# Performance work log

Measured on AMD Instinct MI355X. Metric: run time of the kernel, lower is better.

The kernel has to match this reference:

```python
import jax, jax.numpy as jnp
import numpy as np

L = 4        # number of GCN layers
B = 1024     # batch of brain graphs
R = 116      # ROIs (AAL atlas)
EPS = 1e-5   # BatchNorm eps


def setup_inputs() -> dict:
    key = jax.random.key(0)
    ks = jax.random.split(key, 20)
    def rn(k, shape, scale=0.1):
        return jax.random.normal(k, shape, dtype=jnp.float32) * scale
    return {
        "X": jax.random.normal(ks[0], (B, R, 3), dtype=jnp.float32),
        "Z": jax.random.normal(ks[1], (B, R, R), dtype=jnp.float32),
        "aw1": rn(ks[2], (L, 3, 3)), "ab1": rn(ks[3], (L, 3)),
        "aw2": rn(ks[4], (L, R, R)), "ab2": rn(ks[5], (L, R)),
        "nw": rn(ks[6], (L, 3, 3)), "nb": rn(ks[7], (L, 3)),
        "ew": rn(ks[8], (L, R, R)), "eb": rn(ks[9], (L, R)),
        "gn_g": jnp.ones((L, R), jnp.float32), "gn_b": jnp.zeros((L, R), jnp.float32),
        "ge_g": jnp.ones((L, R), jnp.float32), "ge_b": jnp.zeros((L, R), jnp.float32),
        "dn_w": rn(ks[10], (L + 1, 3)), "dn_b": rn(ks[11], (L + 1,)),
        "dn_g": jnp.ones((L + 1,), jnp.float32), "dn_beta": jnp.zeros((L + 1,), jnp.float32),
        "de_w": rn(ks[12], (L + 1, 78)), "de_b": rn(ks[13], (L + 1,)),
        "de_g": jnp.ones((L + 1,), jnp.float32), "de_beta": jnp.zeros((L + 1,), jnp.float32),
        "cw1": rn(ks[14], (1024, R * 4 * (L + 1)), 0.02), "cb1": jnp.zeros((1024,), jnp.float32),
        "cw2": rn(ks[15], (2, 1024), 0.02), "cb2": jnp.zeros((2,), jnp.float32),
    }


def _bn3(x, g, b):
    # BatchNorm1d(C) in training mode on (N, C, L): stats over (N, L) per channel
    m = x.mean(axis=(0, 2), keepdims=True)
    v = x.var(axis=(0, 2), keepdims=True)
    return (x - m) * jax.lax.rsqrt(v + EPS) * g[None, :, None] + b[None, :, None]


def _down_node(X, w, b, g, beta):
    # ConvDownSample(3): Conv1d(1,1,3) on (B*R,1,3) -> scalar per row, ReLU, BatchNorm1d(1)
    f = jax.nn.relu(X.reshape(-1, 3) @ w + b)                 # (B*R,)
    h = (f - f.mean()) * jax.lax.rsqrt(f.var() + EPS) * g + beta
    return h.reshape(X.shape[0], -1)                          # (B, R)


def _down_edge(Z, w, b, g, beta):
    # ConvDownSample(116): Conv1d(1,1,78,stride=39,pad=39) -> 3 outputs per row
    x = Z.reshape(-1, R)
    xp = jnp.pad(x, ((0, 0), (39, 39)))                       # (B*R, 194)
    win = jnp.stack([xp[:, 39 * t: 39 * t + 78] for t in range(3)], axis=1)  # (B*R,3,78)
    f = jax.nn.relu(win @ w + b)                              # (B*R, 3)
    h = (f - f.mean()) * jax.lax.rsqrt(f.var() + EPS) * g + beta
    return h.reshape(Z.shape[0], -1)                          # (B, 3R)


def reference(X, Z, aw1, ab1, aw2, ab2, nw, nb, ew, eb, gn_g, gn_b, ge_g, ge_b,
              dn_w, dn_b, dn_g, dn_beta, de_w, de_b, de_g, de_beta,
              cw1, cb1, cw2, cb2):
    xx = [_down_node(X, dn_w[0], dn_b[0], dn_g[0], dn_beta[0])]
    zz = [_down_edge(Z, de_w[0], de_b[0], de_g[0], de_beta[0])]
    for i in range(L):
        # Attention: K = conv1(X^T) (1x1 conv == matmul), Q = K^T, scores = Q@K
        K = jnp.einsum('oc,bnc->bon', aw1[i], X) + ab1[i][None, :, None]   # (B,3,R)
        att = jax.nn.softmax(jnp.einsum('bcn,bcm->bnm', K, K), axis=-1)    # (B,R,R)
        V = jnp.einsum('oc,bmc->bom', aw2[i], Z) + ab2[i][None, :, None]   # (B,R,R)
        A = jnp.einsum('bnk,bkm->bmn', att, V)                             # bmm + permute
        # Edge update
        Z1 = jnp.einsum('bnm,bmc->bnc', A, Z) @ ew[i].T + eb[i]
        Z = jax.nn.relu(_bn3(Z1, ge_g[i], ge_b[i])) + Z
        zz.append(_down_edge(Z, de_w[i + 1], de_b[i + 1], de_g[i + 1], de_beta[i + 1]))
        # Node update
        X1 = jnp.einsum('bnm,bmc->bnc', A, X) @ nw[i].T + nb[i]
        X = jax.nn.relu(_bn3(X1, gn_g[i], gn_b[i])) + X
        xx.append(_down_node(X, dn_w[i + 1], dn_b[i + 1], dn_g[i + 1], dn_beta[i + 1]))
    XZ = jnp.concatenate(xx + zz, axis=1)                     # (B, 116*4*(L+1))
    h = jax.nn.relu(XZ @ cw1.T + cb1)                         # dropout is identity (eval)
    return h @ cw2.T + cb2                                    # (B, 2)
```

## Files before the change

### kernel.cpp

```cpp
#include <hip/hip_runtime.h>
#if __has_include(<hip/hip_bf16.h>)
#include <hip/hip_bf16.h>
#define HAVE_HIP_BF16 1
#endif

#define R 116
#define RP 120
#define GZ 13920
#define BATCH 1024
#define NL 4
#define RR2 13456
#define EPSF 1e-5f
#define NZP_ELEM (BATCH * GZ)
#define NZ_ELEM (BATCH * RR2)
#define NX_ELEM (BATCH * R * 3)
#define LS 136
#define XZS 2336
#define NSH 8
#define STL 464
#define NCHP 1740

typedef unsigned short ushort_t;
typedef __attribute__((ext_vector_type(8))) short bf16x8;
typedef __attribute__((ext_vector_type(4))) float f32x4;

__device__ __forceinline__ float bf2f(unsigned short u){
  union { unsigned int i; float f; } v; v.i = ((unsigned int)u) << 16; return v.f;
}
__device__ __forceinline__ unsigned short f2bf(float f){
#ifdef HAVE_HIP_BF16
  union { __hip_bfloat16 h; unsigned short u; } cv;
  cv.h = __float2bfloat16(f);
  return cv.u;
#else
  union { float ff; unsigned int i; } v; v.ff = f;
  return (unsigned short)((v.i + 0x7fffu + ((v.i >> 16) & 1u)) >> 16);
#endif
}
__device__ __forceinline__ float u2f_lo(unsigned w){
  union { unsigned i; float f; } v; v.i = w << 16; return v.f;
}
__device__ __forceinline__ float u2f_hi(unsigned w){
  union { unsigned i; float f; } v; v.i = w & 0xffff0000u; return v.f;
}
__device__ __forceinline__ float wsum(float v){
  #pragma unroll
  for (int o = 32; o > 0; o >>= 1) v += __shfl_xor(v, o, 64);
  return v;
}
__device__ __forceinline__ float wmaxr(float v){
  #pragma unroll
  for (int o = 32; o > 0; o >>= 1) v = fmaxf(v, __shfl_xor(v, o, 64));
  return v;
}

__global__ void k_init(const float* __restrict__ Zin, ushort_t* __restrict__ Zcp,
                       const float* __restrict__ Xin, float* __restrict__ Xc,
                       float* __restrict__ st, unsigned* __restrict__ xzw,
                       unsigned* __restrict__ z1g,
                       const float* __restrict__ aw2, const float* __restrict__ ew,
                       ushort_t* __restrict__ aw2p, ushort_t* __restrict__ ewp,
                       const float* __restrict__ cw1, ushort_t* __restrict__ cw1p,
                       const float* __restrict__ cb2, float* __restrict__ out)
{
  int idx = blockIdx.x * 256 + threadIdx.x;
  int stride = gridDim.x * 256;
  for (int i = idx; i < BATCH * NCHP; i += stride){
    int g = i / NCHP, ch = i - g * NCHP;
    int e0 = ch << 3, r = e0 / RP, c0 = e0 - r * RP;
    const float* zi = Zin + (size_t)g * RR2 + r * R + c0;
    float4 f0 = *(const float4*)zi;
    uint4 w;
    w.x = (unsigned)f2bf(f0.x) | ((unsigned)f2bf(f0.y) << 16);
    w.y = (unsigned)f2bf(f0.z) | ((unsigned)f2bf(f0.w) << 16);
    if (c0 == 112){ w.z = 0u; w.w = 0u; }
    else {
      float4 f1 = *(const float4*)(zi + 4);
      w.z = (unsigned)f2bf(f1.x) | ((unsigned)f2bf(f1.y) << 16);
      w.w = (unsigned)f2bf(f1.z) | ((unsigned)f2bf(f1.w) << 16);
    }
    *(uint4*)(Zcp + (size_t)g * GZ + e0) = w;
  }
  for (int i = idx; i < 1024 * XZS; i += stride){
    int n = i / XZS, k = i - n * XZS;
    cw1p[i] = (k < 2320) ? f2bf(cw1[n*2320 + k]) : (ushort_t)0;
  }
  for (int i = idx; i < 4*128*128; i += stride){
    int l = i >> 14, rem = i & 16383, row = rem >> 7, col = rem & 127;
    ushort_t v = 0, w = 0;
    if (row < R && col < R){
      v = f2bf(aw2[l*RR2 + col*R + row]);
      w = f2bf(ew [l*RR2 + row*R + col]);
    }
    aw2p[i] = v;
    ewp [i] = w;
  }
  for (int i = idx; i < NX_ELEM; i += stride) Xc[i] = Xin[i];
  for (int i = idx; i < 15008; i += stride) st[i] = 0.f;
  for (int i = idx; i < BATCH*XZS/2; i += stride) xzw[i] = 0u;
  for (int i = idx; i < 736; i += stride) z1g[i] = 0u;
  for (int i = idx; i < 1024; i += stride){ out[2*i] = cb2[0]; out[2*i+1] = cb2[1]; }
}

__launch_bounds__(1024, 8)
__global__ void k_fused(float* __restrict__ Xc, ushort_t* __restrict__ Zc,
                        ushort_t* __restrict__ Z1, float* __restrict__ X1,
                        const float* __restrict__ aw1, const float* __restrict__ ab1,
                        const ushort_t* __restrict__ aw2p, const float* __restrict__ ab2,
                        const float* __restrict__ nw,  const float* __restrict__ nb,
                        const ushort_t* __restrict__ ewp,  const float* __restrict__ eb,
                        float* __restrict__ zsumS, float* __restrict__ zsqS,
                        float* __restrict__ xsumS, float* __restrict__ xsqS,
                        const float* __restrict__ geg, const float* __restrict__ geb,
                        const float* __restrict__ gng, const float* __restrict__ gnb,
                        const float* __restrict__ dnw, const float* __restrict__ dnb,
                        const float* __restrict__ dew, const float* __restrict__ deb,
                        ushort_t* __restrict__ XZ,
                        float* __restrict__ dnS, float* __restrict__ deS,
                        int layer, int with_attn)
{
  __shared__ __align__(16) ushort_t bA[128*LS];
  __shared__ __align__(16) ushort_t bB[128*LS];
  __shared__ float Ksm[3*R];
  __shared__ float ssm[R];
  __shared__ float xp[R*12];
  __shared__ float zps[128*2];
  __shared__ float zpq[128*2];
  __shared__ float wsm[78];
  __shared__ float xsred[3], xqred[3];
  __shared__ float zds[8], zqs[8];

  float* zcoA = xp;
  float* zcoC = xp + 116;
  float* xcoA = xp + 232;
  float* xcoC = xp + 348;
  ushort_t* bBlin = bB;

  const int b    = blockIdx.x;
  const int tid  = threadIdx.x;
  const int lane = tid & 63;
  const int wave = tid >> 6;
  const int qm   = lane & 15;
  const int quad = lane >> 4;
  const int tr   = wave & 7;
  const int tc0  = (wave >> 3) * 4;
  const int t_snap = layer;
  const int sh   = b & (NSH-1);

  ushort_t* Zb = Zc + (size_t)b * GZ;
  const ushort_t* Z1b = Z1 + (size_t)b * RR2;
  const float* ab2l = ab2 + layer * R;
  const float* ebl  = eb  + layer * R;
  const float* nwl  = nw  + layer * 9;
  const float* nbl  = nb  + layer * 3;
  const ushort_t* aw2l = aw2p + layer * 16384;
  const ushort_t* ewl  = ewp  + layer * 16384;

  const f32x4 vzero = {0.f, 0.f, 0.f, 0.f};

  if (tid < R){
    float a = 0.f, c = 0.f;
    if (layer > 0){
      const int pl = layer - 1;
      float ms = 0.f, qs = 0.f;
      #pragma unroll
      for (int s2 = 0; s2 < NSH; s2++){
        ms += zsumS[s2*STL + pl*R + tid];
        qs += zsqS [s2*STL + pl*R + tid];
      }
      const float cnt = (float)(BATCH * R);
      float m  = ms / cnt;
      float va = fmaxf(qs / cnt - m*m, 0.f);
      float rs = rsqrtf(va + EPSF);
      a = rs * geg[pl*R + tid];
      c = geb[pl*R + tid] - m * a;
    }
    zcoA[tid] = a; zcoC[tid] = c;
  } else if (tid >= 128 && tid < 128 + R){
    const int r = tid - 128;
    float a = 0.f, c = 0.f;
    if (layer > 0){
      const int pl = layer - 1;
      float ms = 0.f, qs = 0.f;
      #pragma unroll
      for (int s2 = 0; s2 < NSH; s2++){
        ms += xsumS[s2*STL + pl*R + r];
        qs += xsqS [s2*STL + pl*R + r];
      }
      const float cnt = (float)(BATCH * 3);
      float m  = ms / cnt;
      float va = fmaxf(qs / cnt - m*m, 0.f);
      float rs = rsqrtf(va + EPSF);
      a = rs * gng[pl*R + r];
      c = gnb[pl*R + r] - m * a;
    }
    xcoA[r] = a; xcoC[r] = c;
  } else if (tid >= 256 && tid < 256 + 78){
    wsm[tid - 256] = dew[t_snap*78 + (tid - 256)];
  }
  __syncthreads();

  {
    const int ch0 = tid;
    const int ch1 = tid + 1024;
    const bool hasB = (ch1 < NCHP);
    const int e0A = ch0 << 3;
    const int e0B = ch1 << 3;
    uint4 zcA = *(const uint4*)(Zb + e0A);
    uint4 zcB; if (hasB) zcB = *(const uint4*)(Zb + e0B);
    if (layer > 0){
      const int rA = e0A / RP, cA0 = e0A - rA*RP;
      const int rB = hasB ? (e0B / RP) : 0, cB0 = hasB ? (e0B - rB*RP) : 0;
      const ushort_t* z1pA = Z1b + rA*R + cA0;
      const ushort_t* z1pB = Z1b + rB*R + cB0;
      unsigned z1A[4], z1B[4];
      #pragma unroll
      for (int i = 0; i < 4; i++) z1A[i] = *(const unsigned*)(z1pA + 2*i);
      if (hasB){
        #pragma unroll
        for (int i = 0; i < 4; i++) z1B[i] = *(const unsigned*)(z1pB + 2*i);
      }
      #pragma unroll
      for (int half = 0; half < 2; half++){
        if (half == 1 && !hasB) break;
        const int e0 = half ? e0B : e0A;
        const int r  = half ? rB  : rA;
        const int c0 = half ? cB0 : cA0;
        const uint4 zc4 = half ? zcB : zcA;
        const unsigned* z1w = half ? z1B : z1A;
        const float aa = zcoA[r], cc = zcoC[r];
        const unsigned zw[4] = {zc4.x, zc4.y, zc4.z, zc4.w};
        unsigned ow[4];
        #pragma unroll
        for (int h = 0; h < 4; h++){
          float vL = fmaxf(u2f_lo(z1w[h])*aa + cc, 0.f) + u2f_lo(zw[h]);
          float vH = fmaxf(u2f_hi(z1w[h])*aa + cc, 0.f) + u2f_hi(zw[h]);
          ow[h] = (unsigned)f2bf(vL) | ((unsigned)f2bf(vH) << 16);
        }
        if (c0 == 112){ ow[2] = 0u; ow[3] = 0u; }
        uint4 o; o.x = ow[0]; o.y = ow[1]; o.z = ow[2]; o.w = ow[3];
        if (with_attn) *(uint4*)(Zb + e0) = o;
        *(uint4*)&bBlin[e0] = o;
      }
    } else {
      *(uint4*)&bBlin[e0A] = zcA;
      if (hasB) *(uint4*)&bBlin[e0B] = zcB;
    }
  }
  {
    float fv = 0.f;
    if (tid >= 658 && tid < 658 + R){
      const int u = tid - 658;
      float* xcr = Xc + ((size_t)b*R + u)*3;
      float v0, v1, v2;
      if (layer > 0){
        float a = xcoA[u], c = xcoC[u];
        const float* x1r = X1 + ((size_t)b*R + u)*3;
        v0 = fmaxf(x1r[0]*a + c, 0.f) + xcr[0];
        v1 = fmaxf(x1r[1]*a + c, 0.f) + xcr[1];
        v2 = fmaxf(x1r[2]*a + c, 0.f) + xcr[2];
        if (with_attn){ xcr[0] = v0; xcr[1] = v1; xcr[2] = v2; }
      } else {
        v0 = xcr[0]; v1 = xcr[1]; v2 = xcr[2];
      }
      if (with_attn){
        const float* aw1l = aw1 + layer * 9;
        const float* ab1l = ab1 + layer * 3;
        #pragma unroll
        for (int o = 0; o < 3; o++)
          Ksm[o*R + u] = ab1l[o] + aw1l[o*3+0]*v0 + aw1l[o*3+1]*v1 + aw1l[o*3+2]*v2;
      }
      float f = fmaxf(dnw[t_snap*3+0]*v0 + dnw[t_snap*3+1]*v1 + dnw[t_snap*3+2]*v2 + dnb[t_snap], 0.f);
      XZ[(size_t)b*XZS + t_snap*R + u] = f2bf(f);
      fv = f;
    }
    if (wave >= 10 && wave <= 12){
      float s = wsum(fv), q = wsum(fv*fv);
      if (lane == 0){ xsred[wave - 10] = s; xqred[wave - 10] = q; }
    }
  }
  if (tid >= 774){
    for (int i = tid - 774; i < 12*LS; i += 250) bA[116*LS + i] = 0;
    for (int i = tid - 774; i < 116*20; i += 250){
      int r = i/20, c = 116 + (i - r*20);
      bA[r*LS + c] = 0;
    }
  }
  __syncthreads();

  if (wave < 10){
    if (tid == 0){
      atomicAdd(&dnS[sh*10 + t_snap*2+0], xsred[0] + xsred[1] + xsred[2]);
      atomicAdd(&dnS[sh*10 + t_snap*2+1], xqred[0] + xqred[1] + xqred[2]);
    }
    if (with_attn){
      for (int n = wave; n < R; n += 10){
        float k0 = Ksm[n], k1 = Ksm[R+n], k2 = Ksm[2*R+n];
        int m0 = lane, m1 = lane + 64;
        float a0 = k0*Ksm[m0] + k1*Ksm[R+m0] + k2*Ksm[2*R+m0];
        float a1 = (m1 < R) ? (k0*Ksm[m1] + k1*Ksm[R+m1] + k2*Ksm[2*R+m1]) : -1e30f;
        float mx = wmaxr(fmaxf(a0, a1));
        float e0 = __expf(a0 - mx);
        float e1 = (m1 < R) ? __expf(a1 - mx) : 0.f;
        float sm = wsum(e0 + e1);
        float sab = wsum(e0 * ab2l[m0] + ((m1 < R) ? e1 * ab2l[m1] : 0.f));
        float inv = 1.f / sm;
        bA[n*LS + m0] = f2bf(e0 * inv);
        if (m1 < R) bA[n*LS + m1] = f2bf(e1 * inv);
        if (lane == 0) ssm[n] = sab * inv;
      }
    }
  } else {
    const int u = tid - 640;
    float f = 0.f;
    if (u < 348){
      int r = u / 3, w = u - 3*r;
      int jlo = (w == 0) ? 39 : 0;
      int jhi = (w == 2) ? 77 : 78;
      int off = (w - 1) * 39;
      const ushort_t* vr = &bBlin[r*RP];
      float acc = 0.f;
      for (int j = jlo; j < jhi; j++) acc += wsm[j] * bf2f(vr[j + off]);
      f = fmaxf(acc + deb[t_snap], 0.f);
      XZ[(size_t)b*XZS + 5*R + t_snap*3*R + r*3 + w] = f2bf(f);
    }
    float s = wsum(f), q = wsum(f*f);
    if (lane == 0){ zds[wave - 10] = s; zqs[wave - 10] = q; }
  }
  __syncthreads();

  if (tid == 0){
    float ss = 0.f, qq = 0.f;
    #pragma unroll
    for (int k = 0; k < 6; k++){ ss += zds[k]; qq += zqs[k]; }
    atomicAdd(&deS[sh*10 + t_snap*2+0], ss);
    atomicAdd(&deS[sh*10 + t_snap*2+1], qq);
  }
  if (!with_attn) return;

  {
    f32x4 acc[4];
    #pragma unroll
    for (int t = 0; t < 4; t++) acc[t] = vzero;
    for (int kk = 0; kk < 128; kk += 32){
      bf16x8 a = *(const bf16x8*)(aw2l + (tr*16 + qm)*128 + kk + quad*8);
      #pragma unroll
      for (int t = 0; t < 4; t++){
        bf16x8 bf = *(const bf16x8*)&bA[((tc0 + t)*16 + qm)*LS + kk + quad*8];
        acc[t] = __builtin_amdgcn_mfma_f32_16x16x32_bf16(a, bf, acc[t], 0, 0, 0);
      }
    }
    const int r0 = tr*16 + quad*4;
    #pragma unroll
    for (int t = 0; t < 4; t++){
      int nn = (tc0 + t)*16 + qm;
      uint2 w;
      w.x = (unsigned)f2bf(acc[t][0]) | ((unsigned)f2bf(acc[t][1]) << 16);
      w.y = (unsigned)f2bf(acc[t][2]) | ((unsigned)f2bf(acc[t][3]) << 16);
      *(uint2*)&bB[nn*LS + r0] = w;
    }
  }
  __syncthreads();

  {
    f32x4 acc[4];
    #pragma unroll
    for (int t = 0; t < 4; t++) acc[t] = vzero;
    for (int kk = 0; kk < 128; kk += 32){
      bf16x8 a = *(const bf16x8*)&bB[(tr*16 + qm)*LS + kk + quad*8];
      #pragma unroll
      for (int t = 0; t < 4; t++){
        int nn = (tc0 + t)*16 + qm;
        bf16x8 bf = *(const bf16x8*)(Zb + nn*RP + kk + quad*8);
        acc[t] = __builtin_amdgcn_mfma_f32_16x16x32_bf16(a, bf, acc[t], 0, 0, 0);
      }
    }
    const int r0 = tr*16 + quad*4;
    float s0 = 0.f, s1 = 0.f, s2 = 0.f, s3 = 0.f;
    if (r0 < R){ s0 = ssm[r0]; s1 = ssm[r0+1]; s2 = ssm[r0+2]; s3 = ssm[r0+3]; }
    #pragma unroll
    for (int t = 0; t < 4; t++){
      int nn = (tc0 + t)*16 + qm;
      uint2 w;
      w.x = (unsigned)f2bf(acc[t][0] + s0) | ((unsigned)f2bf(acc[t][1] + s1) << 16);
      w.y = (unsigned)f2bf(acc[t][2] + s2) | ((unsigned)f2bf(acc[t][3] + s3) << 16);
      *(uint2*)&bA[nn*LS + r0] = w;
    }
  }
  __syncthreads();

  {
    f32x4 acc[4];
    #pragma unroll
    for (int t = 0; t < 4; t++) acc[t] = vzero;
    for (int kk = 0; kk < 128; kk += 32){
      bf16x8 a = *(const bf16x8*)(Zb + (tr*16 + qm)*RP + kk + quad*8);
      #pragma unroll
      for (int t = 0; t < 4; t++){
        bf16x8 bf = *(const bf16x8*)(ewl + ((tc0 + t)*16 + qm)*128 + kk + quad*8);
        acc[t] = __builtin_amdgcn_mfma_f32_16x16x32_bf16(a, bf, acc[t], 0, 0, 0);
      }
    }
    const int r0 = tr*16 + quad*4;
    #pragma unroll
    for (int t = 0; t < 4; t++){
      int nn = (tc0 + t)*16 + qm;
      uint2 w;
      w.x = (unsigned)f2bf(acc[t][0]) | ((unsigned)f2bf(acc[t][1]) << 16);
      w.y = (unsigned)f2bf(acc[t][2]) | ((unsigned)f2bf(acc[t][3]) << 16);
      *(uint2*)&bB[nn*LS + r0] = w;
    }
  }
  __syncthreads();

  {
    f32x4 acc[4];
    #pragma unroll
    for (int t = 0; t < 4; t++) acc[t] = vzero;
    for (int kk = 0; kk < 128; kk += 32){
      bf16x8 a = *(const bf16x8*)&bA[(tr*16 + qm)*LS + kk + quad*8];
      #pragma unroll
      for (int t = 0; t < 4; t++){
        bf16x8 bf = *(const bf16x8*)&bB[((tc0 + t)*16 + qm)*LS + kk + quad*8];
        acc[t] = __builtin_amdgcn_mfma_f32_16x16x32_bf16(a, bf, acc[t], 0, 0, 0);
      }
    }
    float ssv[4] = {0.f,0.f,0.f,0.f}, sqv[4] = {0.f,0.f,0.f,0.f};
    #pragma unroll
    for (int t = 0; t < 4; t++){
      int col = (tc0 + t)*16 + qm;
      float bias = (col < R) ? ebl[col] : 0.f;
      #pragma unroll
      for (int rg = 0; rg < 4; rg++){
        int row = tr*16 + quad*4 + rg;
        float v = (col < R) ? (acc[t][rg] + bias) : 0.f;
        if (col < R && row < R)
          Z1[(size_t)b*RR2 + row*R + col] = f2bf(v);
        ssv[rg] += v; sqv[rg] += v*v;
      }
    }
    #pragma unroll
    for (int off = 1; off < 16; off <<= 1){
      #pragma unroll
      for (int rg = 0; rg < 4; rg++){
        ssv[rg] += __shfl_xor(ssv[rg], off, 64);
        sqv[rg] += __shfl_xor(sqv[rg], off, 64);
      }
    }
    if (qm == 0){
      int half = wave >> 3;
      #pragma unroll
      for (int rg = 0; rg < 4; rg++){
        int row = tr*16 + quad*4 + rg;
        zps[row*2 + half] = ssv[rg];
        zpq[row*2 + half] = sqv[rg];
      }
    }
  }

  const float* Xb = Xc + (size_t)b * R * 3;
  if (tid < R*4){
    int n = tid >> 2, part = tid & 3;
    const ushort_t* rowp = &bA[n*LS];
    float t0 = 0.f, t1 = 0.f, t2 = 0.f;
    for (int mb = part*4; mb < 116; mb += 16){
      uint2 w = *(const uint2*)(rowp + mb);
      float p0 = u2f_lo(w.x), p1 = u2f_hi(w.x), p2 = u2f_lo(w.y), p3 = u2f_hi(w.y);
      const float* x4 = Xb + mb*3;
      t0 = fmaf(p0, x4[0], fmaf(p1, x4[3], fmaf(p2, x4[6], fmaf(p3, x4[9],  t0))));
      t1 = fmaf(p0, x4[1], fmaf(p1, x4[4], fmaf(p2, x4[7], fmaf(p3, x4[10], t1))));
      t2 = fmaf(p0, x4[2], fmaf(p1, x4[5], fmaf(p2, x4[8], fmaf(p3, x4[11], t2))));
    }
    xp[tid*3+0] = t0; xp[tid*3+1] = t1; xp[tid*3+2] = t2;
  }
  __syncthreads();
  if (tid < R){
    float c0 = xp[tid*12+0] + xp[tid*12+3] + xp[tid*12+6] + xp[tid*12+9];
    float c1 = xp[tid*12+1] + xp[tid*12+4] + xp[tid*12+7] + xp[tid*12+10];
    float c2 = xp[tid*12+2] + xp[tid*12+5] + xp[tid*12+8] + xp[tid*12+11];
    float s = 0.f, q = 0.f;
    #pragma unroll
    for (int e = 0; e < 3; e++){
      float v = nbl[e] + c0*nwl[e*3+0] + c1*nwl[e*3+1] + c2*nwl[e*3+2];
      X1[((size_t)b*R + tid)*3 + e] = v;
      s += v; q += v*v;
    }
    atomicAdd(&xsumS[sh*STL + layer*R + tid], s);
    atomicAdd(&xsqS [sh*STL + layer*R + tid], q);
    atomicAdd(&zsumS[sh*STL + layer*R + tid], zps[tid*2] + zps[tid*2+1]);
    atomicAdd(&zsqS [sh*STL + layer*R + tid], zpq[tid*2] + zpq[tid*2+1]);
  }
}

__global__ void k_applyAll(const float* __restrict__ dnS, const float* __restrict__ deS,
                           const float* __restrict__ dng, const float* __restrict__ dnbe,
                           const float* __restrict__ deg, const float* __restrict__ debe,
                           ushort_t* __restrict__ XZ)
{
  int idx = blockIdx.x * 256 + threadIdx.x;
  int bi = idx / R, r = idx - bi*R;
  const float cn = (float)(BATCH * R);
  const float ce = (float)(BATCH * R * 3);
  #pragma unroll
  for (int t = 0; t < 5; t++){
    float dns = 0.f, dnq = 0.f, des = 0.f, deq = 0.f;
    #pragma unroll
    for (int s2 = 0; s2 < NSH; s2++){
      dns += dnS[s2*10 + t*2+0]; dnq += dnS[s2*10 + t*2+1];
      des += deS[s2*10 + t*2+0]; deq += deS[s2*10 + t*2+1];
    }
    float mn = dns / cn;
    float vn = fmaxf(dnq / cn - mn*mn, 0.f);
    size_t sn = (size_t)bi*XZS + t*R + r;
    float hn = (bf2f(XZ[sn]) - mn) * rsqrtf(vn + EPSF) * dng[t] + dnbe[t];
    XZ[sn] = f2bf(hn);
    float me = des / ce;
    float ve = fmaxf(deq / ce - me*me, 0.f);
    float rse = rsqrtf(ve + EPSF);
    size_t se = (size_t)bi*XZS + 5*R + t*3*R + r*3;
    #pragma unroll
    for (int p = 0; p < 3; p++){
      float he = (bf2f(XZ[se+p]) - me) * rse * deg[t] + debe[t];
      XZ[se+p] = f2bf(he);
    }
  }
}

__launch_bounds__(256)
__global__ void k_fc(const ushort_t* __restrict__ XZ, const ushort_t* __restrict__ cw1p,
                     const float* __restrict__ cb1, const float* __restrict__ cw2,
                     float* __restrict__ out){
  const int tid  = threadIdx.x;
  const int lane = tid & 63;
  const int wave = tid >> 6;
  const int qm   = lane & 15;
  const int quad = lane >> 4;
  const int m0   = blockIdx.x * 64 + wave * 16;
  const int n0   = blockIdx.y * 64;

  const f32x4 vzero = {0.f, 0.f, 0.f, 0.f};
  f32x4 acc[4];
  #pragma unroll
  for (int t = 0; t < 4; t++) acc[t] = vzero;

  const ushort_t* arow = XZ + (size_t)(m0 + qm) * XZS;
  for (int kk = 0; kk < XZS; kk += 32){
    bf16x8 a = *(const bf16x8*)(arow + kk + quad*8);
    #pragma unroll
    for (int t = 0; t < 4; t++){
      const ushort_t* brow = cw1p + (size_t)(n0 + t*16 + qm) * XZS;
      bf16x8 bf = *(const bf16x8*)(brow + kk + quad*8);
      acc[t] = __builtin_amdgcn_mfma_f32_16x16x32_bf16(a, bf, acc[t], 0, 0, 0);
    }
  }
  #pragma unroll
  for (int rg = 0; rg < 4; rg++){
    float p0 = 0.f, p1 = 0.f;
    #pragma unroll
    for (int t = 0; t < 4; t++){
      int n = n0 + t*16 + qm;
      float h = fmaxf(acc[t][rg] + cb1[n], 0.f);
      p0 = fmaf(h, cw2[n], p0);
      p1 = fmaf(h, cw2[1024 + n], p1);
    }
    #pragma unroll
    for (int o = 1; o < 16; o <<= 1){
      p0 += __shfl_xor(p0, o, 64);
      p1 += __shfl_xor(p1, o, 64);
    }
    if (qm == 0){
      int m = m0 + quad*4 + rg;
      atomicAdd(&out[m*2 + 0], p0);
      atomicAdd(&out[m*2 + 1], p1);
    }
  }
}

extern "C" void kernel_launch(void* const* d_in, const int* in_sizes, int n_in,
                              void* d_out, int out_size, void* d_ws, size_t ws_size,
                              hipStream_t stream)
{
  const float* Xin  = (const float*)d_in[0];
  const float* Zin  = (const float*)d_in[1];
  const float* aw1  = (const float*)d_in[2];
  const float* ab1  = (const float*)d_in[3];
  const float* aw2  = (const float*)d_in[4];
  const float* ab2  = (const float*)d_in[5];
  const float* nw   = (const float*)d_in[6];
  const float* nb   = (const float*)d_in[7];
  const float* ew   = (const float*)d_in[8];
  const float* eb   = (const float*)d_in[9];
  const float* gng  = (const float*)d_in[10];
  const float* gnb  = (const float*)d_in[11];
  const float* geg  = (const float*)d_in[12];
  const float* geb  = (const float*)d_in[13];
  const float* dnw  = (const float*)d_in[14];
  const float* dnb  = (const float*)d_in[15];
  const float* dng  = (const float*)d_in[16];
  const float* dnbe = (const float*)d_in[17];
  const float* dew  = (const float*)d_in[18];
  const float* deb  = (const float*)d_in[19];
  const float* deg  = (const float*)d_in[20];
  const float* debe = (const float*)d_in[21];
  const float* cw1  = (const float*)d_in[22];
  const float* cb1  = (const float*)d_in[23];
  const float* cw2  = (const float*)d_in[24];
  const float* cb2  = (const float*)d_in[25];

  ushort_t* Zc = (ushort_t*)d_ws;
  ushort_t* Z1 = Zc + NZP_ELEM;
  float*    Xc = (float*)(Z1 + NZ_ELEM);
  float*    X1 = Xc + NX_ELEM;
  ushort_t* XZ = (ushort_t*)(X1 + NX_ELEM);
  float*    st = (float*)(XZ + BATCH*XZS);
  float* zsumS = st;
  float* zsqS  = st + 3712;
  float* xsumS = st + 7424;
  float* xsqS  = st + 11136;
  float* dnS   = st + 14848;
  float* deS   = st + 14928;
  ushort_t* aw2p = (ushort_t*)(st + 15008);
  ushort_t* ewp  = aw2p + 4*16384;
  ushort_t* cw1p = ewp + 4*16384;

  float* outp = (float*)d_out;

  k_init<<<4096, 256, 0, stream>>>(Zin, Zc, Xin, Xc,
                                   st, (unsigned*)XZ, (unsigned*)Z1,
                                   aw2, ew, aw2p, ewp, cw1, cw1p, cb2, outp);

  for (int i = 0; i < NL; i++){
    k_fused<<<BATCH, 1024, 0, stream>>>(Xc, Zc, Z1, X1, aw1, ab1, aw2p, ab2,
                                        nw, nb, ewp, eb, zsumS, zsqS, xsumS, xsqS,
                                        geg, geb, gng, gnb, dnw, dnb, dew, deb,
                                        XZ, dnS, deS, i, 1);
  }
  k_fused<<<BATCH, 1024, 0, stream>>>(Xc, Zc, Z1, X1, aw1, ab1, aw2p, ab2,
                                      nw, nb, ewp, eb, zsumS, zsqS, xsumS, xsqS,
                                      geg, geb, gng, gnb, dnw, dnb, dew, deb,
                                      XZ, dnS, deS, NL, 0);

  k_applyAll<<<464, 256, 0, stream>>>(dnS, deS, dng, dnbe, deg, debe, XZ);

  k_fc<<<dim3(16, 16), 256, 0, stream>>>(XZ, cw1p, cb1, cw2, outp);
}
```

Measured before the change: 653.3 us.

## Prefetch layer inputs before stats sync, fold snapshot BN into final fused pass

Global loads of Z, Z1 and the X rows move ahead of the statistics-reduction prologue and its barrier, so their latency overlaps with the BN coefficient computation. The final fused pass (no attention) now also applies BatchNorm to snapshots 0-3 of the XZ buffer, leaving only snapshot 4 for the separate apply kernel. Nontemporal loads and stores are used for the Z conversion in init and for the Z1 streams. The cost is higher register pressure from holding the prefetched data across the barrier in a 1024-thread block.

```diff
diff --git a/kernel.cpp b/kernel.cpp
--- a/kernel.cpp
+++ b/kernel.cpp
@@ -23,6 +23,8 @@
 typedef unsigned short ushort_t;
 typedef __attribute__((ext_vector_type(8))) short bf16x8;
 typedef __attribute__((ext_vector_type(4))) float f32x4;
+typedef __attribute__((ext_vector_type(4))) float fvec4;
+typedef __attribute__((ext_vector_type(4))) unsigned uvec4;
 
 __device__ __forceinline__ float bf2f(unsigned short u){
   union { unsigned int i; float f; } v; v.i = ((unsigned int)u) << 16; return v.f;
@@ -69,17 +71,17 @@
     int g = i / NCHP, ch = i - g * NCHP;
     int e0 = ch << 3, r = e0 / RP, c0 = e0 - r * RP;
     const float* zi = Zin + (size_t)g * RR2 + r * R + c0;
-    float4 f0 = *(const float4*)zi;
-    uint4 w;
+    fvec4 f0 = __builtin_nontemporal_load((const fvec4*)zi);
+    uvec4 w;
     w.x = (unsigned)f2bf(f0.x) | ((unsigned)f2bf(f0.y) << 16);
     w.y = (unsigned)f2bf(f0.z) | ((unsigned)f2bf(f0.w) << 16);
     if (c0 == 112){ w.z = 0u; w.w = 0u; }
     else {
-      float4 f1 = *(const float4*)(zi + 4);
+      fvec4 f1 = __builtin_nontemporal_load((const fvec4*)(zi + 4));
       w.z = (unsigned)f2bf(f1.x) | ((unsigned)f2bf(f1.y) << 16);
       w.w = (unsigned)f2bf(f1.z) | ((unsigned)f2bf(f1.w) << 16);
     }
-    *(uint4*)(Zcp + (size_t)g * GZ + e0) = w;
+    __builtin_nontemporal_store(w, (uvec4*)(Zcp + (size_t)g * GZ + e0));
   }
   for (int i = idx; i < 1024 * XZS; i += stride){
     int n = i / XZS, k = i - n * XZS;
@@ -115,6 +117,8 @@
                         const float* __restrict__ gng, const float* __restrict__ gnb,
                         const float* __restrict__ dnw, const float* __restrict__ dnb,
                         const float* __restrict__ dew, const float* __restrict__ deb,
+                        const float* __restrict__ dng, const float* __restrict__ dnbe,
+                        const float* __restrict__ deg, const float* __restrict__ debe,
                         ushort_t* __restrict__ XZ,
                         float* __restrict__ dnS, float* __restrict__ deS,
                         int layer, int with_attn)
@@ -158,6 +162,38 @@
 
   const f32x4 vzero = {0.f, 0.f, 0.f, 0.f};
 
+  const int ch1 = tid + 1024;
+  const bool hasB = (ch1 < NCHP);
+  const int e0A = tid << 3;
+  const int e0B = ch1 << 3;
+  const int rA = e0A / RP, cA0 = e0A - rA*RP;
+  const int rB = hasB ? (e0B / RP) : 0, cB0 = hasB ? (e0B - rB*RP) : 0;
+  uint4 zcA, zcB;
+  unsigned z1A[4] = {0u,0u,0u,0u}, z1B[4] = {0u,0u,0u,0u};
+  zcA = *(const uint4*)(Zb + e0A);
+  if (hasB) zcB = *(const uint4*)(Zb + e0B);
+  if (layer > 0){
+    const ushort_t* z1pA = Z1b + rA*R + cA0;
+    #pragma unroll
+    for (int i = 0; i < 4; i++) z1A[i] = __builtin_nontemporal_load((const unsigned*)(z1pA + 2*i));
+    if (hasB){
+      const ushort_t* z1pB = Z1b + rB*R + cB0;
+      #pragma unroll
+      for (int i = 0; i < 4; i++) z1B[i] = __builtin_nontemporal_load((const unsigned*)(z1pB + 2*i));
+    }
+  }
+  const bool isXrow = (tid >= 658 && tid < 658 + R);
+  float ex0=0.f, ex1=0.f, ex2=0.f, exc0=0.f, exc1=0.f, exc2=0.f;
+  if (isXrow){
+    const float* xcr = Xc + ((size_t)b*R + (tid-658))*3;
+    exc0 = xcr[0]; exc1 = xcr[1]; exc2 = xcr[2];
+    if (layer > 0){
+      const float* x1r = X1 + ((size_t)b*R + (tid-658))*3;
+      ex0 = x1r[0]; ex1 = x1r[1]; ex2 = x1r[2];
+    }
+  }
+  asm volatile("" ::: "memory");
+
   if (tid < R){
     float a = 0.f, c = 0.f;
     if (layer > 0){
@@ -200,68 +236,49 @@
   }
   __syncthreads();
 
-  {
-    const int ch0 = tid;
-    const int ch1 = tid + 1024;
-    const bool hasB = (ch1 < NCHP);
-    const int e0A = ch0 << 3;
-    const int e0B = ch1 << 3;
-    uint4 zcA = *(const uint4*)(Zb + e0A);
-    uint4 zcB; if (hasB) zcB = *(const uint4*)(Zb + e0B);
-    if (layer > 0){
-      const int rA = e0A / RP, cA0 = e0A - rA*RP;
-      const int rB = hasB ? (e0B / RP) : 0, cB0 = hasB ? (e0B - rB*RP) : 0;
-      const ushort_t* z1pA = Z1b + rA*R + cA0;
-      const ushort_t* z1pB = Z1b + rB*R + cB0;
-      unsigned z1A[4], z1B[4];
-      #pragma unroll
-      for (int i = 0; i < 4; i++) z1A[i] = *(const unsigned*)(z1pA + 2*i);
-      if (hasB){
-        #pragma unroll
-        for (int i = 0; i < 4; i++) z1B[i] = *(const unsigned*)(z1pB + 2*i);
-      }
-      #pragma unroll
-      for (int half = 0; half < 2; half++){
-        if (half == 1 && !hasB) break;
-        const int e0 = half ? e0B : e0A;
-        const int r  = half ? rB  : rA;
-        const int c0 = half ? cB0 : cA0;
-        const uint4 zc4 = half ? zcB : zcA;
-        const unsigned* z1w = half ? z1B : z1A;
-        const float aa = zcoA[r], cc = zcoC[r];
-        const unsigned zw[4] = {zc4.x, zc4.y, zc4.z, zc4.w};
-        unsigned ow[4];
-        #pragma unroll
-        for (int h = 0; h < 4; h++){
-          float vL = fmaxf(u2f_lo(z1w[h])*aa + cc, 0.f) + u2f_lo(zw[h]);
-          float vH = fmaxf(u2f_hi(z1w[h])*aa + cc, 0.f) + u2f_hi(zw[h]);
-          ow[h] = (unsigned)f2bf(vL) | ((unsigned)f2bf(vH) << 16);
-        }
-        if (c0 == 112){ ow[2] = 0u; ow[3] = 0u; }
-        uint4 o; o.x = ow[0]; o.y = ow[1]; o.z = ow[2]; o.w = ow[3];
-        if (with_attn) *(uint4*)(Zb + e0) = o;
-        *(uint4*)&bBlin[e0] = o;
-      }
-    } else {
-      *(uint4*)&bBlin[e0A] = zcA;
-      if (hasB) *(uint4*)&bBlin[e0B] = zcB;
-    }
+  if (layer > 0){
+    #pragma unroll
+    for (int half = 0; half < 2; half++){
+      if (half == 1 && !hasB) break;
+      const int e0 = half ? e0B : e0A;
+      const int r  = half ? rB  : rA;
+      const int c0 = half ? cB0 : cA0;
+      const uint4 zc4 = half ? zcB : zcA;
+      const unsigned* z1w = half ? z1B : z1A;
+      const float aa = zcoA[r], cc = zcoC[r];
+      const unsigned zw[4] = {zc4.x, zc4.y, zc4.z, zc4.w};
+      unsigned ow[4];
+      #pragma unroll
+      for (int h = 0; h < 4; h++){
+        float vL = fmaxf(u2f_lo(z1w[h])*aa + cc, 0.f) + u2f_lo(zw[h]);
+        float vH = fmaxf(u2f_hi(z1w[h])*aa + cc, 0.f) + u2f_hi(zw[h]);
+        ow[h] = (unsigned)f2bf(vL) | ((unsigned)f2bf(vH) << 16);
+      }
+      if (c0 == 112){ ow[2] = 0u; ow[3] = 0u; }
+      uint4 o; o.x = ow[0]; o.y = ow[1]; o.z = ow[2]; o.w = ow[3];
+      if (with_attn) *(uint4*)(Zb + e0) = o;
+      *(uint4*)&bBlin[e0] = o;
+    }
+  } else {
+    *(uint4*)&bBlin[e0A] = zcA;
+    if (hasB) *(uint4*)&bBlin[e0B] = zcB;
   }
   {
     float fv = 0.f;
-    if (tid >= 658 && tid < 658 + R){
+    if (isXrow){
       const int u = tid - 658;
-      float* xcr = Xc + ((size_t)b*R + u)*3;
       float v0, v1, v2;
       if (layer > 0){
         float a = xcoA[u], c = xcoC[u];
-        const float* x1r = X1 + ((size_t)b*R + u)*3;
-        v0 = fmaxf(x1r[0]*a + c, 0.f) + xcr[0];
-        v1 = fmaxf(x1r[1]*a + c, 0.f) + xcr[1];
-        v2 = fmaxf(x1r[2]*a + c, 0.f) + xcr[2];
-        if (with_attn){ xcr[0] = v0; xcr[1] = v1; xcr[2] = v2; }
+        v0 = fmaxf(ex0*a + c, 0.f) + exc0;
+        v1 = fmaxf(ex1*a + c, 0.f) + exc1;
+        v2 = fmaxf(ex2*a + c, 0.f) + exc2;
+        if (with_attn){
+          float* xcr = Xc + ((size_t)b*R + u)*3;
+          xcr[0] = v0; xcr[1] = v1; xcr[2] = v2;
+        }
       } else {
-        v0 = xcr[0]; v1 = xcr[1]; v2 = xcr[2];
+        v0 = exc0; v1 = exc1; v2 = exc2;
       }
       if (with_attn){
         const float* aw1l = aw1 + layer * 9;
@@ -336,7 +353,43 @@
     atomicAdd(&deS[sh*10 + t_snap*2+0], ss);
     atomicAdd(&deS[sh*10 + t_snap*2+1], qq);
   }
-  if (!with_attn) return;
+  if (!with_attn){
+    if (tid < 464){
+      if (tid < R){
+        const float cn = (float)(BATCH * R);
+        size_t base = (size_t)b*XZS + tid;
+        #pragma unroll
+        for (int t = 0; t < 4; t++){
+          float ms = 0.f, qs = 0.f;
+          #pragma unroll
+          for (int s2 = 0; s2 < NSH; s2++){ ms += dnS[s2*10 + t*2+0]; qs += dnS[s2*10 + t*2+1]; }
+          float mn = ms / cn;
+          float vn = fmaxf(qs / cn - mn*mn, 0.f);
+          float a = rsqrtf(vn + EPSF) * dng[t];
+          float c = dnbe[t] - mn * a;
+          size_t sn = base + (size_t)t*R;
+          XZ[sn] = f2bf(bf2f(XZ[sn]) * a + c);
+        }
+      } else {
+        const int v = tid - R;
+        const float ce = (float)(BATCH * R * 3);
+        size_t base = (size_t)b*XZS + 5*R + v;
+        #pragma unroll
+        for (int t = 0; t < 4; t++){
+          float ms = 0.f, qs = 0.f;
+          #pragma unroll
+          for (int s2 = 0; s2 < NSH; s2++){ ms += deS[s2*10 + t*2+0]; qs += deS[s2*10 + t*2+1]; }
+          float me = ms / ce;
+          float ve = fmaxf(qs / ce - me*me, 0.f);
+          float a = rsqrtf(ve + EPSF) * deg[t];
+          float c = debe[t] - me * a;
+          size_t se = base + (size_t)t*3*R;
+          XZ[se] = f2bf(bf2f(XZ[se]) * a + c);
+        }
+      }
+    }
+    return;
+  }
 
   {
     f32x4 acc[4];
@@ -435,7 +488,7 @@
         int row = tr*16 + quad*4 + rg;
         float v = (col < R) ? (acc[t][rg] + bias) : 0.f;
         if (col < R && row < R)
-          Z1[(size_t)b*RR2 + row*R + col] = f2bf(v);
+          __builtin_nontemporal_store(f2bf(v), &Z1[(size_t)b*RR2 + row*R + col]);
         ssv[rg] += v; sqv[rg] += v*v;
       }
     }
@@ -492,38 +545,32 @@
   }
 }
 
-__global__ void k_applyAll(const float* __restrict__ dnS, const float* __restrict__ deS,
-                           const float* __restrict__ dng, const float* __restrict__ dnbe,
-                           const float* __restrict__ deg, const float* __restrict__ debe,
-                           ushort_t* __restrict__ XZ)
+__global__ void k_apply4(const float* __restrict__ dnS, const float* __restrict__ deS,
+                         const float* __restrict__ dng, const float* __restrict__ dnbe,
+                         const float* __restrict__ deg, const float* __restrict__ debe,
+                         ushort_t* __restrict__ XZ)
 {
   int idx = blockIdx.x * 256 + threadIdx.x;
   int bi = idx / R, r = idx - bi*R;
   const float cn = (float)(BATCH * R);
   const float ce = (float)(BATCH * R * 3);
+  float dns = 0.f, dnq = 0.f, des = 0.f, deq = 0.f;
   #pragma unroll
-  for (int t = 0; t < 5; t++){
-    float dns = 0.f, dnq = 0.f, des = 0.f, deq = 0.f;
-    #pragma unroll
-    for (int s2 = 0; s2 < NSH; s2++){
-      dns += dnS[s2*10 + t*2+0]; dnq += dnS[s2*10 + t*2+1];
-      des += deS[s2*10 + t*2+0]; deq += deS[s2*10 + t*2+1];
-    }
-    float mn = dns / cn;
-    float vn = fmaxf(dnq / cn - mn*mn, 0.f);
-    size_t sn = (size_t)bi*XZS + t*R + r;
-    float hn = (bf2f(XZ[sn]) - mn) * rsqrtf(vn + EPSF) * dng[t] + dnbe[t];
-    XZ[sn] = f2bf(hn);
-    float me = des / ce;
-    float ve = fmaxf(deq / ce - me*me, 0.f);
-    float rse = rsqrtf(ve + EPSF);
-    size_t se = (size_t)bi*XZS + 5*R + t*3*R + r*3;
-    #pragma unroll
-    for (int p = 0; p < 3; p++){
-      float he = (bf2f(XZ[se+p]) - me) * rse * deg[t] + debe[t];
-      XZ[se+p] = f2bf(he);
-    }
-  }
+  for (int s2 = 0; s2 < NSH; s2++){
+    dns += dnS[s2*10 + 8]; dnq += dnS[s2*10 + 9];
+    des += deS[s2*10 + 8]; deq += deS[s2*10 + 9];
+  }
+  float mn = dns / cn;
+  float vn = fmaxf(dnq / cn - mn*mn, 0.f);
+  size_t sn = (size_t)bi*XZS + 4*R + r;
+  XZ[sn] = f2bf((bf2f(XZ[sn]) - mn) * rsqrtf(vn + EPSF) * dng[4] + dnbe[4]);
+  float me = des / ce;
+  float ve = fmaxf(deq / ce - me*me, 0.f);
+  float rse = rsqrtf(ve + EPSF);
+  size_t se = (size_t)bi*XZS + 5*R + 4*3*R + r*3;
+  #pragma unroll
+  for (int p = 0; p < 3; p++)
+    XZ[se+p] = f2bf((bf2f(XZ[se+p]) - me) * rse * deg[4] + debe[4]);
 }
 
 __launch_bounds__(256)
@@ -633,14 +680,16 @@
     k_fused<<<BATCH, 1024, 0, stream>>>(Xc, Zc, Z1, X1, aw1, ab1, aw2p, ab2,
                                         nw, nb, ewp, eb, zsumS, zsqS, xsumS, xsqS,
                                         geg, geb, gng, gnb, dnw, dnb, dew, deb,
+                                        dng, dnbe, deg, debe,
                                         XZ, dnS, deS, i, 1);
   }
   k_fused<<<BATCH, 1024, 0, stream>>>(Xc, Zc, Z1, X1, aw1, ab1, aw2p, ab2,
                                       nw, nb, ewp, eb, zsumS, zsqS, xsumS, xsqS,
                                       geg, geb, gng, gnb, dnw, dnb, dew, deb,
+                                      dng, dnbe, deg, debe,
                                       XZ, dnS, deS, NL, 0);
 
-  k_applyAll<<<464, 256, 0, stream>>>(dnS, deS, dng, dnbe, deg, debe, XZ);
+  k_apply4<<<464, 256, 0, stream>>>(dnS, deS, dng, dnbe, deg, debe, XZ);
 
   k_fc<<<dim3(16, 16), 256, 0, stream>>>(XZ, cw1p, cb1, cw2, outp);
 }
```

Result: slower. 706.5 us (+8.1%).
